# Kernel optimization log

Measured on AMD Instinct MI355X. Metric: run time of the kernel, lower is better.

Reference implementation:

```python
import jax, jax.numpy as jnp
import numpy as np

B, T, E = 8, 1024, 1024
H, HS = 16, 64  # num_heads, head_size; H*HS == E


def setup_inputs() -> dict:
    key = jax.random.key(0)
    k1, k2, k3, k4, k5, k6 = jax.random.split(key, 6)
    x = jax.random.normal(k1, (B, T, E), dtype=jnp.float32)
    s = E ** -0.5
    Wk = jax.random.normal(k2, (H, HS, E), dtype=jnp.float32) * s
    Wq = jax.random.normal(k3, (H, HS, E), dtype=jnp.float32) * s
    Wv = jax.random.normal(k4, (H, HS, E), dtype=jnp.float32) * s
    Wproj = jax.random.normal(k5, (E, E), dtype=jnp.float32) * s
    i = 0
    return {"x": x, "Wk": Wk, "Wq": Wq, "Wv": Wv, "Wproj": Wproj, "i": i}


def reference(x, Wk, Wq, Wv, Wproj, i):
    # choices fixed at full supernet config: embed_dim=E, head_size=HS, no biases.
    b, t, e = x.shape
    hs = Wk.shape[1]
    # per-head projections, heads batched: [B,H,T,HS]
    k = jnp.einsum('bte,hde->bhtd', x, Wk)
    q = jnp.einsum('bte,hde->bhtd', x, Wq)
    v = jnp.einsum('bte,hde->bhtd', x, Wv)
    wei = jnp.einsum('bhtd,bhsd->bhts', q, k) * (hs ** -0.5)  # [B,H,T,T]
    causal = jnp.tril(jnp.ones((t, t), dtype=bool))
    wei = jnp.where(causal, wei, -jnp.inf)
    wei = jax.nn.softmax(wei, axis=-1)  # dropout p=0 (eval)
    out = jnp.einsum('bhts,bhsd->bthd', wei, v).reshape(b, t, -1)  # concat heads
    out = out @ Wproj.T  # proj, bias_proj=False
    return out
```

## Files before the change

### kernel.cpp

```cpp
#include <hip/hip_runtime.h>

#define B_  8
#define T_  1024
#define E_  1024
#define H_  16
#define HS_ 64
#define K_  1024

typedef __bf16 bf16x8 __attribute__((ext_vector_type(8)));
typedef float  f32x4  __attribute__((ext_vector_type(4)));
typedef unsigned short us;

__device__ __forceinline__ us f2bf(float f) {
    union { float f; unsigned int i; } c; c.f = f;
    unsigned int x = c.i;
    return (us)((x + 0x7fff + ((x >> 16) & 1)) >> 16);
}
__device__ __forceinline__ us f2bf_t(float f) {
    union { float f; unsigned int i; } c; c.f = f;
    return (us)(c.i >> 16);
}
__device__ __forceinline__ bf16x8 cvt8(const float* p) {
    float4 a = *reinterpret_cast<const float4*>(p);
    float4 b = *reinterpret_cast<const float4*>(p + 4);
    union { bf16x8 v; us u[8]; } c;
    c.u[0] = f2bf(a.x); c.u[1] = f2bf(a.y); c.u[2] = f2bf(a.z); c.u[3] = f2bf(a.w);
    c.u[4] = f2bf(b.x); c.u[5] = f2bf(b.y); c.u[6] = f2bf(b.z); c.u[7] = f2bf(b.w);
    return c.v;
}
__device__ __forceinline__ void async_cp16(const us* g, us* l) {
    __builtin_amdgcn_global_load_lds((const unsigned int*)g, (unsigned int*)l, 16, 0, 0);
}

__global__ __launch_bounds__(256) void cvt_kernel(
    const float* __restrict__ sx, const float* __restrict__ sq,
    const float* __restrict__ sk, const float* __restrict__ sv,
    const float* __restrict__ sp,
    us* __restrict__ dx, us* __restrict__ dq, us* __restrict__ dk,
    us* __restrict__ dv, us* __restrict__ dp)
{
    const int y = blockIdx.y;
    const float* src = (y == 0) ? sx : (y == 1) ? sq : (y == 2) ? sk : (y == 3) ? sv : sp;
    us*          dst = (y == 0) ? dx : (y == 1) ? dq : (y == 2) ? dk : (y == 3) ? dv : dp;
    const size_t n = (y == 0) ? (size_t)B_ * T_ * E_ : (size_t)E_ * E_;
    const size_t i = ((size_t)blockIdx.x * 256 + threadIdx.x) * 8;
    if (i >= n) return;
    *reinterpret_cast<bf16x8*>(dst + i) = cvt8(src + i);
}

__global__ __launch_bounds__(256) void qkv_gf(
    const us* __restrict__ A,
    const us* __restrict__ Wq, const us* __restrict__ Wk, const us* __restrict__ Wv,
    us* __restrict__ q, us* __restrict__ k, us* __restrict__ vT)
{
    const int type = blockIdx.z;
    const us* Bm = (type == 0) ? Wq : (type == 1) ? Wk : Wv;
    us* out      = (type == 0) ? q  : (type == 1) ? k  : vT;
    const int vtrans = (type == 2);

    __shared__ __align__(16) us As[128 * 64];
    __shared__ __align__(16) us Bs[128 * 64];

    const int tid  = threadIdx.x;
    const int lane = tid & 63;
    const int w    = tid >> 6;
    const int quad = lane >> 4;
    const int l15  = lane & 15;
    const int wm   = w >> 1, wn = w & 1;
    const int row0 = blockIdx.x * 128;
    const int col0 = blockIdx.y * 128;
    const int x7   = l15 & 7;
    const int ca0  = (quad ^ x7) * 8;
    const int ca1  = ((4 + quad) ^ x7) * 8;

    const us* pa[4]; const us* pb[4];
#pragma unroll
    for (int i = 0; i < 4; ++i) {
        const int idx = tid + i * 256;
        const int r   = idx >> 3;
        const int c8  = ((idx & 7) ^ (r & 7)) * 8;
        pa[i] = A  + (size_t)(row0 + r) * K_ + c8;
        pb[i] = Bm + (size_t)(col0 + r) * K_ + c8;
    }

    f32x4 acc[4][4] = {};
    for (int k0 = 0; k0 < K_; k0 += 64) {
        __syncthreads();
#pragma unroll
        for (int i = 0; i < 4; ++i) {
            async_cp16(pa[i], &As[(tid + i * 256) * 8]);
            async_cp16(pb[i], &Bs[(tid + i * 256) * 8]);
            pa[i] += 64; pb[i] += 64;
        }
        __syncthreads();
#pragma unroll
        for (int kk = 0; kk < 2; ++kk) {
            const int ca = kk ? ca1 : ca0;
            bf16x8 af[4], bf[4];
#pragma unroll
            for (int t = 0; t < 4; ++t) {
                af[t] = *reinterpret_cast<const bf16x8*>(&As[(wm * 64 + t * 16 + l15) * 64 + ca]);
                bf[t] = *reinterpret_cast<const bf16x8*>(&Bs[(wn * 64 + t * 16 + l15) * 64 + ca]);
            }
#pragma unroll
            for (int mt = 0; mt < 4; ++mt)
#pragma unroll
                for (int nt = 0; nt < 4; ++nt)
                    acc[mt][nt] = __builtin_amdgcn_mfma_f32_16x16x32_bf16(af[mt], bf[nt], acc[mt][nt], 0, 0, 0);
        }
    }

#pragma unroll
    for (int mt = 0; mt < 4; ++mt)
#pragma unroll
        for (int nt = 0; nt < 4; ++nt)
#pragma unroll
            for (int r = 0; r < 4; ++r) {
                const int m = row0 + wm * 64 + mt * 16 + quad * 4 + r;
                const int n = col0 + wn * 64 + nt * 16 + l15;
                const int b = m >> 10, t = m & 1023;
                const int h = n >> 6,  d = n & 63;
                const us vb = f2bf(acc[mt][nt][r]);
                if (vtrans)  out[((size_t)((b * 16 + h) * 64 + d)) * 1024 + t] = vb;
                else         out[((size_t)(b * 16 + h) * 1024 + t) * 64 + d] = vb;
            }
}

__global__ __launch_bounds__(256) void proj_gf(
    const us* __restrict__ A, const us* __restrict__ Bm, float* __restrict__ C)
{
    __shared__ __align__(16) us As[128 * 64];
    __shared__ __align__(16) us Bs[128 * 64];

    const int tid  = threadIdx.x;
    const int lane = tid & 63;
    const int w    = tid >> 6;
    const int quad = lane >> 4;
    const int l15  = lane & 15;
    const int wm   = w >> 1, wn = w & 1;
    const int row0 = blockIdx.x * 128;
    const int col0 = blockIdx.y * 128;
    const int x7   = l15 & 7;
    const int ca0  = (quad ^ x7) * 8;
    const int ca1  = ((4 + quad) ^ x7) * 8;

    const us* pa[4]; const us* pb[4];
#pragma unroll
    for (int i = 0; i < 4; ++i) {
        const int idx = tid + i * 256;
        const int r   = idx >> 3;
        const int c8  = ((idx & 7) ^ (r & 7)) * 8;
        pa[i] = A  + (size_t)(row0 + r) * K_ + c8;
        pb[i] = Bm + (size_t)(col0 + r) * K_ + c8;
    }

    f32x4 acc[4][4] = {};
    for (int k0 = 0; k0 < K_; k0 += 64) {
        __syncthreads();
#pragma unroll
        for (int i = 0; i < 4; ++i) {
            async_cp16(pa[i], &As[(tid + i * 256) * 8]);
            async_cp16(pb[i], &Bs[(tid + i * 256) * 8]);
            pa[i] += 64; pb[i] += 64;
        }
        __syncthreads();
#pragma unroll
        for (int kk = 0; kk < 2; ++kk) {
            const int ca = kk ? ca1 : ca0;
            bf16x8 af[4], bf[4];
#pragma unroll
            for (int t = 0; t < 4; ++t) {
                af[t] = *reinterpret_cast<const bf16x8*>(&As[(wm * 64 + t * 16 + l15) * 64 + ca]);
                bf[t] = *reinterpret_cast<const bf16x8*>(&Bs[(wn * 64 + t * 16 + l15) * 64 + ca]);
            }
#pragma unroll
            for (int mt = 0; mt < 4; ++mt)
#pragma unroll
                for (int nt = 0; nt < 4; ++nt)
                    acc[mt][nt] = __builtin_amdgcn_mfma_f32_16x16x32_bf16(af[mt], bf[nt], acc[mt][nt], 0, 0, 0);
        }
    }

#pragma unroll
    for (int mt = 0; mt < 4; ++mt)
#pragma unroll
        for (int nt = 0; nt < 4; ++nt)
#pragma unroll
            for (int r = 0; r < 4; ++r) {
                const int m = row0 + wm * 64 + mt * 16 + quad * 4 + r;
                const int n = col0 + wn * 64 + nt * 16 + l15;
                C[(size_t)m * E_ + n] = acc[mt][nt][r];
            }
}

#define CSCALE 0.18033688011112042f

__global__ __launch_bounds__(256) void attn_v8(
    const us* __restrict__ Q, const us* __restrict__ K,
    const us* __restrict__ VT, us* __restrict__ O)
{
    const int px = blockIdx.x;
    const int bh = blockIdx.y;
    const int tA = px, tB = 15 - px;
    const size_t base  = (size_t)bh * T_ * HS_;
    const size_t baseT = (size_t)bh * HS_ * T_;
    const int tid  = threadIdx.x;
    const int w    = tid >> 6;
    const int lane = tid & 63;
    const int quad = lane >> 4;
    const int l15  = lane & 15;

    __shared__ __align__(16) us kt[64][72];
    __shared__ __align__(16) us vt[64][72];
    __shared__ __align__(16) us psA[4][16][72];
    __shared__ __align__(16) us psB[4][16][72];

    const int rowA = tA * 64 + w * 16;
    const int rowB = tB * 64 + w * 16;

    bf16x8 qfA0, qfA1, qfB0, qfB1;
    {
        const us* qa = Q + base + (size_t)(rowA + l15) * HS_ + quad * 8;
        const us* qb = Q + base + (size_t)(rowB + l15) * HS_ + quad * 8;
        qfA0 = *reinterpret_cast<const bf16x8*>(qa);
        qfA1 = *reinterpret_cast<const bf16x8*>(qa + 32);
        qfB0 = *reinterpret_cast<const bf16x8*>(qb);
        qfB1 = *reinterpret_cast<const bf16x8*>(qb + 32);
    }

    const int sr0 = tid >> 3;
    const int sc0 = (tid & 7) * 8;
    const int sr1 = sr0 + 32;

    const us* kp0 = K + base + (size_t)sr0 * HS_ + sc0;
    const us* kp1 = K + base + (size_t)sr1 * HS_ + sc0;
    const us* vp0 = VT + baseT + (size_t)sr0 * T_ + sc0;
    const us* vp1 = VT + baseT + (size_t)sr1 * T_ + sc0;

    float lA[4] = {0.f, 0.f, 0.f, 0.f}, lB[4] = {0.f, 0.f, 0.f, 0.f};
    f32x4 oA[4] = {}, oB[4] = {};

    bf16x8 kr0, kr1, vr0, vr1;
    kr0 = *reinterpret_cast<const bf16x8*>(kp0);
    kr1 = *reinterpret_cast<const bf16x8*>(kp1);
    vr0 = *reinterpret_cast<const bf16x8*>(vp0);
    vr1 = *reinterpret_cast<const bf16x8*>(vp1);

    const int nch = tB + 1;
    for (int ch = 0; ch < nch; ++ch) {
        const int s0 = ch * 64;
        const bool actA = (ch <= tA);

        __syncthreads();
        *reinterpret_cast<bf16x8*>(&kt[sr0][sc0]) = kr0;
        *reinterpret_cast<bf16x8*>(&kt[sr1][sc0]) = kr1;
        *reinterpret_cast<bf16x8*>(&vt[sr0][sc0]) = vr0;
        *reinterpret_cast<bf16x8*>(&vt[sr1][sc0]) = vr1;
        __syncthreads();

        if (ch + 1 < nch) {
            kp0 += 64 * HS_; kp1 += 64 * HS_; vp0 += 64; vp1 += 64;
            kr0 = *reinterpret_cast<const bf16x8*>(kp0);
            kr1 = *reinterpret_cast<const bf16x8*>(kp1);
            vr0 = *reinterpret_cast<const bf16x8*>(vp0);
            vr1 = *reinterpret_cast<const bf16x8*>(vp1);
        }

        f32x4 sA[4] = {}, sB[4] = {};
#pragma unroll
        for (int nt = 0; nt < 4; ++nt) {
            bf16x8 kf0 = *reinterpret_cast<const bf16x8*>(&kt[nt * 16 + l15][quad * 8]);
            bf16x8 kf1 = *reinterpret_cast<const bf16x8*>(&kt[nt * 16 + l15][quad * 8 + 32]);
            sB[nt] = __builtin_amdgcn_mfma_f32_16x16x32_bf16(qfB0, kf0, sB[nt], 0, 0, 0);
            sB[nt] = __builtin_amdgcn_mfma_f32_16x16x32_bf16(qfB1, kf1, sB[nt], 0, 0, 0);
            if (actA) {
                sA[nt] = __builtin_amdgcn_mfma_f32_16x16x32_bf16(qfA0, kf0, sA[nt], 0, 0, 0);
                sA[nt] = __builtin_amdgcn_mfma_f32_16x16x32_bf16(qfA1, kf1, sA[nt], 0, 0, 0);
            }
        }
        if (ch == tB) {
#pragma unroll
            for (int nt = 0; nt < 4; ++nt)
#pragma unroll
                for (int r = 0; r < 4; ++r)
                    if (s0 + nt * 16 + l15 > rowB + quad * 4 + r) sB[nt][r] = -1e30f;
        }
        if (ch == tA) {
#pragma unroll
            for (int nt = 0; nt < 4; ++nt)
#pragma unroll
                for (int r = 0; r < 4; ++r)
                    if (s0 + nt * 16 + l15 > rowA + quad * 4 + r) sA[nt][r] = -1e30f;
        }

#pragma unroll
        for (int r = 0; r < 4; ++r)
#pragma unroll
            for (int nt = 0; nt < 4; ++nt) {
                const float pB = exp2f(sB[nt][r] * CSCALE);
                lB[r] += pB;
                psB[w][quad * 4 + r][nt * 16 + l15] = f2bf_t(pB);
            }
        if (actA) {
#pragma unroll
            for (int r = 0; r < 4; ++r)
#pragma unroll
                for (int nt = 0; nt < 4; ++nt) {
                    const float pA = exp2f(sA[nt][r] * CSCALE);
                    lA[r] += pA;
                    psA[w][quad * 4 + r][nt * 16 + l15] = f2bf_t(pA);
                }
        }

        bf16x8 pfB0 = *reinterpret_cast<const bf16x8*>(&psB[w][l15][quad * 8]);
        bf16x8 pfB1 = *reinterpret_cast<const bf16x8*>(&psB[w][l15][quad * 8 + 32]);
        bf16x8 pfA0, pfA1;
        if (actA) {
            pfA0 = *reinterpret_cast<const bf16x8*>(&psA[w][l15][quad * 8]);
            pfA1 = *reinterpret_cast<const bf16x8*>(&psA[w][l15][quad * 8 + 32]);
        }

#pragma unroll
        for (int dt = 0; dt < 4; ++dt) {
            bf16x8 vf0 = *reinterpret_cast<const bf16x8*>(&vt[dt * 16 + l15][quad * 8]);
            bf16x8 vf1 = *reinterpret_cast<const bf16x8*>(&vt[dt * 16 + l15][quad * 8 + 32]);
            oB[dt] = __builtin_amdgcn_mfma_f32_16x16x32_bf16(pfB0, vf0, oB[dt], 0, 0, 0);
            oB[dt] = __builtin_amdgcn_mfma_f32_16x16x32_bf16(pfB1, vf1, oB[dt], 0, 0, 0);
            if (actA) {
                oA[dt] = __builtin_amdgcn_mfma_f32_16x16x32_bf16(pfA0, vf0, oA[dt], 0, 0, 0);
                oA[dt] = __builtin_amdgcn_mfma_f32_16x16x32_bf16(pfA1, vf1, oA[dt], 0, 0, 0);
            }
        }
    }

#pragma unroll
    for (int r = 0; r < 4; ++r) {
#pragma unroll
        for (int off = 1; off < 16; off <<= 1) {
            lA[r] += __shfl_xor(lA[r], off);
            lB[r] += __shfl_xor(lB[r], off);
        }
    }
    const int b = bh >> 4, h = bh & 15;
#pragma unroll
    for (int r = 0; r < 4; ++r) {
        const float invA = 1.f / lA[r];
        const float invB = 1.f / lB[r];
        const size_t offA = ((size_t)b * T_ + rowA + quad * 4 + r) * E_ + h * HS_;
        const size_t offB = ((size_t)b * T_ + rowB + quad * 4 + r) * E_ + h * HS_;
#pragma unroll
        for (int dt = 0; dt < 4; ++dt) {
            O[offA + dt * 16 + l15] = f2bf(oA[dt][r] * invA);
            O[offB + dt * 16 + l15] = f2bf(oB[dt][r] * invB);
        }
    }
}

extern "C" void kernel_launch(void* const* d_in, const int* in_sizes, int n_in,
                              void* d_out, int out_size, void* d_ws, size_t ws_size,
                              hipStream_t stream) {
    const float* x  = (const float*)d_in[0];
    const float* Wk = (const float*)d_in[1];
    const float* Wq = (const float*)d_in[2];
    const float* Wv = (const float*)d_in[3];
    const float* Wp = (const float*)d_in[4];

    const size_t qe = (size_t)B_ * H_ * T_ * HS_;
    const size_t we = (size_t)E_ * E_;

    us* xb = (us*)d_ws;
    us* wq = xb + qe;
    us* wk = wq + we;
    us* wv = wk + we;
    us* wp = wv + we;
    us* q  = wp + we;
    us* k  = q + qe;
    us* vT = k + qe;
    us* o  = xb;

    cvt_kernel<<<dim3(4096, 5), 256, 0, stream>>>(x, Wq, Wk, Wv, Wp,
                                                  xb, wq, wk, wv, wp);
    qkv_gf<<<dim3(64, 8, 3), 256, 0, stream>>>(xb, wq, wk, wv, q, k, vT);
    attn_v8<<<dim3(8, 128), 256, 0, stream>>>(q, k, vT, o);
    proj_gf<<<dim3(64, 8), 256, 0, stream>>>(o, wp, (float*)d_out);
}
```

Measured before the change: 246.8 us.

## Double-buffer shared memory tiles in QKV and projection GEMMs

Both GEMM kernels now use two shared-memory buffers per operand. Each iteration issues async copies for the next K-tile into the alternate buffer before computing MFMAs on the current one, with a single barrier per iteration instead of two. This aims to hide global-load latency behind compute. Shared memory per block doubles to 64 KB, which may lower occupancy. Correctness depends on the async copy being complete at the barrier.

```diff
diff --git a/kernel.cpp b/kernel.cpp
--- a/kernel.cpp
+++ b/kernel.cpp
@@ -58,8 +58,8 @@
     us* out      = (type == 0) ? q  : (type == 1) ? k  : vT;
     const int vtrans = (type == 2);
 
-    __shared__ __align__(16) us As[128 * 64];
-    __shared__ __align__(16) us Bs[128 * 64];
+    __shared__ __align__(16) us As[2][128 * 64];
+    __shared__ __align__(16) us Bs[2][128 * 64];
 
     const int tid  = threadIdx.x;
     const int lane = tid & 63;
@@ -84,23 +84,32 @@
     }
 
     f32x4 acc[4][4] = {};
-    for (int k0 = 0; k0 < K_; k0 += 64) {
-        __syncthreads();
-#pragma unroll
-        for (int i = 0; i < 4; ++i) {
-            async_cp16(pa[i], &As[(tid + i * 256) * 8]);
-            async_cp16(pb[i], &Bs[(tid + i * 256) * 8]);
-            pa[i] += 64; pb[i] += 64;
-        }
-        __syncthreads();
+#pragma unroll
+    for (int i = 0; i < 4; ++i) {
+        async_cp16(pa[i], &As[0][(tid + i * 256) * 8]);
+        async_cp16(pb[i], &Bs[0][(tid + i * 256) * 8]);
+        pa[i] += 64; pb[i] += 64;
+    }
+    __syncthreads();
+
+    for (int t = 0; t < 16; ++t) {
+        const int cur = t & 1;
+        if (t < 15) {
+#pragma unroll
+            for (int i = 0; i < 4; ++i) {
+                async_cp16(pa[i], &As[cur ^ 1][(tid + i * 256) * 8]);
+                async_cp16(pb[i], &Bs[cur ^ 1][(tid + i * 256) * 8]);
+                pa[i] += 64; pb[i] += 64;
+            }
+        }
 #pragma unroll
         for (int kk = 0; kk < 2; ++kk) {
             const int ca = kk ? ca1 : ca0;
             bf16x8 af[4], bf[4];
 #pragma unroll
-            for (int t = 0; t < 4; ++t) {
-                af[t] = *reinterpret_cast<const bf16x8*>(&As[(wm * 64 + t * 16 + l15) * 64 + ca]);
-                bf[t] = *reinterpret_cast<const bf16x8*>(&Bs[(wn * 64 + t * 16 + l15) * 64 + ca]);
+            for (int tt = 0; tt < 4; ++tt) {
+                af[tt] = *reinterpret_cast<const bf16x8*>(&As[cur][(wm * 64 + tt * 16 + l15) * 64 + ca]);
+                bf[tt] = *reinterpret_cast<const bf16x8*>(&Bs[cur][(wn * 64 + tt * 16 + l15) * 64 + ca]);
             }
 #pragma unroll
             for (int mt = 0; mt < 4; ++mt)
@@ -108,6 +117,7 @@
                 for (int nt = 0; nt < 4; ++nt)
                     acc[mt][nt] = __builtin_amdgcn_mfma_f32_16x16x32_bf16(af[mt], bf[nt], acc[mt][nt], 0, 0, 0);
         }
+        __syncthreads();
     }
 
 #pragma unroll
@@ -129,8 +139,8 @@
 __global__ __launch_bounds__(256) void proj_gf(
     const us* __restrict__ A, const us* __restrict__ Bm, float* __restrict__ C)
 {
-    __shared__ __align__(16) us As[128 * 64];
-    __shared__ __align__(16) us Bs[128 * 64];
+    __shared__ __align__(16) us As[2][128 * 64];
+    __shared__ __align__(16) us Bs[2][128 * 64];
 
     const int tid  = threadIdx.x;
     const int lane = tid & 63;
@@ -155,23 +165,32 @@
     }
 
     f32x4 acc[4][4] = {};
-    for (int k0 = 0; k0 < K_; k0 += 64) {
-        __syncthreads();
-#pragma unroll
-        for (int i = 0; i < 4; ++i) {
-            async_cp16(pa[i], &As[(tid + i * 256) * 8]);
-            async_cp16(pb[i], &Bs[(tid + i * 256) * 8]);
-            pa[i] += 64; pb[i] += 64;
-        }
-        __syncthreads();
+#pragma unroll
+    for (int i = 0; i < 4; ++i) {
+        async_cp16(pa[i], &As[0][(tid + i * 256) * 8]);
+        async_cp16(pb[i], &Bs[0][(tid + i * 256) * 8]);
+        pa[i] += 64; pb[i] += 64;
+    }
+    __syncthreads();
+
+    for (int t = 0; t < 16; ++t) {
+        const int cur = t & 1;
+        if (t < 15) {
+#pragma unroll
+            for (int i = 0; i < 4; ++i) {
+                async_cp16(pa[i], &As[cur ^ 1][(tid + i * 256) * 8]);
+                async_cp16(pb[i], &Bs[cur ^ 1][(tid + i * 256) * 8]);
+                pa[i] += 64; pb[i] += 64;
+            }
+        }
 #pragma unroll
         for (int kk = 0; kk < 2; ++kk) {
             const int ca = kk ? ca1 : ca0;
             bf16x8 af[4], bf[4];
 #pragma unroll
-            for (int t = 0; t < 4; ++t) {
-                af[t] = *reinterpret_cast<const bf16x8*>(&As[(wm * 64 + t * 16 + l15) * 64 + ca]);
-                bf[t] = *reinterpret_cast<const bf16x8*>(&Bs[(wn * 64 + t * 16 + l15) * 64 + ca]);
+            for (int tt = 0; tt < 4; ++tt) {
+                af[tt] = *reinterpret_cast<const bf16x8*>(&As[cur][(wm * 64 + tt * 16 + l15) * 64 + ca]);
+                bf[tt] = *reinterpret_cast<const bf16x8*>(&Bs[cur][(wn * 64 + tt * 16 + l15) * 64 + ca]);
             }
 #pragma unroll
             for (int mt = 0; mt < 4; ++mt)
@@ -179,6 +198,7 @@
                 for (int nt = 0; nt < 4; ++nt)
                     acc[mt][nt] = __builtin_amdgcn_mfma_f32_16x16x32_bf16(af[mt], bf[nt], acc[mt][nt], 0, 0, 0);
         }
+        __syncthreads();
     }
 
 #pragma unroll
```

Result: slower. 254.4 us (+3.1%).

## Keep softmax probabilities in registers by computing transposed scores

Applied to the files above, without the earlier changes.

The QK^T MFMA operands are swapped so each lane holds S^T. The exponentiated probabilities then already sit in the A-operand layout of a 16x16x16 bf16 MFMA for the PV product. This removes the per-warp shared-memory P buffers, along with their store and reload, and the mask and row-sum reduction are adapted to the transposed layout. In exchange, PV uses twice as many narrower K=16 MFMAs and more, smaller V fragment loads from LDS, which may cost matrix-core throughput.

```diff
diff --git a/kernel.cpp b/kernel.cpp
--- a/kernel.cpp
+++ b/kernel.cpp
@@ -8,6 +8,7 @@
 #define K_  1024
 
 typedef __bf16 bf16x8 __attribute__((ext_vector_type(8)));
+typedef __bf16 bf16x4 __attribute__((ext_vector_type(4)));
 typedef float  f32x4  __attribute__((ext_vector_type(4)));
 typedef unsigned short us;
 
@@ -30,6 +31,21 @@
 }
 __device__ __forceinline__ void async_cp16(const us* g, us* l) {
     __builtin_amdgcn_global_load_lds((const unsigned int*)g, (unsigned int*)l, 16, 0, 0);
+}
+
+__device__ __forceinline__ f32x4 mfma_pv16(bf16x4 a, bf16x4 b, f32x4 c) {
+#if __has_builtin(__builtin_amdgcn_mfma_f32_16x16x16_bf16)
+    return __builtin_amdgcn_mfma_f32_16x16x16_bf16(a, b, c, 0, 0, 0);
+#elif __has_builtin(__builtin_amdgcn_mfma_f32_16x16x16bf16_1k)
+    typedef short s16x4 __attribute__((ext_vector_type(4)));
+    union U { bf16x4 b; s16x4 s; };
+    U ua, ub; ua.b = a; ub.b = b;
+    return __builtin_amdgcn_mfma_f32_16x16x16bf16_1k(ua.s, ub.s, c, 0, 0, 0);
+#else
+    f32x4 d = c;
+    asm("v_mfma_f32_16x16x16_bf16 %0, %1, %2, %0" : "+v"(d) : "v"(a), "v"(b));
+    return d;
+#endif
 }
 
 __global__ __launch_bounds__(256) void cvt_kernel(
@@ -195,7 +211,7 @@
 
 #define CSCALE 0.18033688011112042f
 
-__global__ __launch_bounds__(256) void attn_v8(
+__global__ __launch_bounds__(256) void attn_v9(
     const us* __restrict__ Q, const us* __restrict__ K,
     const us* __restrict__ VT, us* __restrict__ O)
 {
@@ -212,8 +228,6 @@
 
     __shared__ __align__(16) us kt[64][72];
     __shared__ __align__(16) us vt[64][72];
-    __shared__ __align__(16) us psA[4][16][72];
-    __shared__ __align__(16) us psB[4][16][72];
 
     const int rowA = tA * 64 + w * 16;
     const int rowB = tB * 64 + w * 16;
@@ -237,7 +251,7 @@
     const us* vp0 = VT + baseT + (size_t)sr0 * T_ + sc0;
     const us* vp1 = VT + baseT + (size_t)sr1 * T_ + sc0;
 
-    float lA[4] = {0.f, 0.f, 0.f, 0.f}, lB[4] = {0.f, 0.f, 0.f, 0.f};
+    float lA = 0.f, lB = 0.f;
     f32x4 oA[4] = {}, oB[4] = {};
 
     bf16x8 kr0, kr1, vr0, vr1;
@@ -271,11 +285,11 @@
         for (int nt = 0; nt < 4; ++nt) {
             bf16x8 kf0 = *reinterpret_cast<const bf16x8*>(&kt[nt * 16 + l15][quad * 8]);
             bf16x8 kf1 = *reinterpret_cast<const bf16x8*>(&kt[nt * 16 + l15][quad * 8 + 32]);
-            sB[nt] = __builtin_amdgcn_mfma_f32_16x16x32_bf16(qfB0, kf0, sB[nt], 0, 0, 0);
-            sB[nt] = __builtin_amdgcn_mfma_f32_16x16x32_bf16(qfB1, kf1, sB[nt], 0, 0, 0);
+            sB[nt] = __builtin_amdgcn_mfma_f32_16x16x32_bf16(kf0, qfB0, sB[nt], 0, 0, 0);
+            sB[nt] = __builtin_amdgcn_mfma_f32_16x16x32_bf16(kf1, qfB1, sB[nt], 0, 0, 0);
             if (actA) {
-                sA[nt] = __builtin_amdgcn_mfma_f32_16x16x32_bf16(qfA0, kf0, sA[nt], 0, 0, 0);
-                sA[nt] = __builtin_amdgcn_mfma_f32_16x16x32_bf16(qfA1, kf1, sA[nt], 0, 0, 0);
+                sA[nt] = __builtin_amdgcn_mfma_f32_16x16x32_bf16(kf0, qfA0, sA[nt], 0, 0, 0);
+                sA[nt] = __builtin_amdgcn_mfma_f32_16x16x32_bf16(kf1, qfA1, sA[nt], 0, 0, 0);
             }
         }
         if (ch == tB) {
@@ -283,69 +297,63 @@
             for (int nt = 0; nt < 4; ++nt)
 #pragma unroll
                 for (int r = 0; r < 4; ++r)
-                    if (s0 + nt * 16 + l15 > rowB + quad * 4 + r) sB[nt][r] = -1e30f;
+                    if (s0 + nt * 16 + quad * 4 + r > rowB + l15) sB[nt][r] = -1e30f;
         }
         if (ch == tA) {
 #pragma unroll
             for (int nt = 0; nt < 4; ++nt)
 #pragma unroll
                 for (int r = 0; r < 4; ++r)
-                    if (s0 + nt * 16 + l15 > rowA + quad * 4 + r) sA[nt][r] = -1e30f;
-        }
-
-#pragma unroll
-        for (int r = 0; r < 4; ++r)
+                    if (s0 + nt * 16 + quad * 4 + r > rowA + l15) sA[nt][r] = -1e30f;
+        }
+
+        bf16x4 paB[4], paA[4];
+#pragma unroll
+        for (int nt = 0; nt < 4; ++nt) {
+            union { bf16x4 v; us u[4]; } pk;
+#pragma unroll
+            for (int r = 0; r < 4; ++r) {
+                const float p = exp2f(sB[nt][r] * CSCALE);
+                lB += p;
+                pk.u[r] = f2bf_t(p);
+            }
+            paB[nt] = pk.v;
+        }
+        if (actA) {
 #pragma unroll
             for (int nt = 0; nt < 4; ++nt) {
-                const float pB = exp2f(sB[nt][r] * CSCALE);
-                lB[r] += pB;
-                psB[w][quad * 4 + r][nt * 16 + l15] = f2bf_t(pB);
-            }
-        if (actA) {
-#pragma unroll
-            for (int r = 0; r < 4; ++r)
-#pragma unroll
-                for (int nt = 0; nt < 4; ++nt) {
-                    const float pA = exp2f(sA[nt][r] * CSCALE);
-                    lA[r] += pA;
-                    psA[w][quad * 4 + r][nt * 16 + l15] = f2bf_t(pA);
+                union { bf16x4 v; us u[4]; } pk;
+#pragma unroll
+                for (int r = 0; r < 4; ++r) {
+                    const float p = exp2f(sA[nt][r] * CSCALE);
+                    lA += p;
+                    pk.u[r] = f2bf_t(p);
                 }
-        }
-
-        bf16x8 pfB0 = *reinterpret_cast<const bf16x8*>(&psB[w][l15][quad * 8]);
-        bf16x8 pfB1 = *reinterpret_cast<const bf16x8*>(&psB[w][l15][quad * 8 + 32]);
-        bf16x8 pfA0, pfA1;
-        if (actA) {
-            pfA0 = *reinterpret_cast<const bf16x8*>(&psA[w][l15][quad * 8]);
-            pfA1 = *reinterpret_cast<const bf16x8*>(&psA[w][l15][quad * 8 + 32]);
+                paA[nt] = pk.v;
+            }
         }
 
 #pragma unroll
         for (int dt = 0; dt < 4; ++dt) {
-            bf16x8 vf0 = *reinterpret_cast<const bf16x8*>(&vt[dt * 16 + l15][quad * 8]);
-            bf16x8 vf1 = *reinterpret_cast<const bf16x8*>(&vt[dt * 16 + l15][quad * 8 + 32]);
-            oB[dt] = __builtin_amdgcn_mfma_f32_16x16x32_bf16(pfB0, vf0, oB[dt], 0, 0, 0);
-            oB[dt] = __builtin_amdgcn_mfma_f32_16x16x32_bf16(pfB1, vf1, oB[dt], 0, 0, 0);
-            if (actA) {
-                oA[dt] = __builtin_amdgcn_mfma_f32_16x16x32_bf16(pfA0, vf0, oA[dt], 0, 0, 0);
-                oA[dt] = __builtin_amdgcn_mfma_f32_16x16x32_bf16(pfA1, vf1, oA[dt], 0, 0, 0);
-            }
-        }
-    }
-
+#pragma unroll
+            for (int nt = 0; nt < 4; ++nt) {
+                const bf16x4 vf = *reinterpret_cast<const bf16x4*>(
+                    &vt[dt * 16 + l15][nt * 16 + quad * 4]);
+                oB[dt] = mfma_pv16(paB[nt], vf, oB[dt]);
+                if (actA) oA[dt] = mfma_pv16(paA[nt], vf, oA[dt]);
+            }
+        }
+    }
+
+    lA += __shfl_xor(lA, 16); lA += __shfl_xor(lA, 32);
+    lB += __shfl_xor(lB, 16); lB += __shfl_xor(lB, 32);
+
+    const int b = bh >> 4, h = bh & 15;
 #pragma unroll
     for (int r = 0; r < 4; ++r) {
-#pragma unroll
-        for (int off = 1; off < 16; off <<= 1) {
-            lA[r] += __shfl_xor(lA[r], off);
-            lB[r] += __shfl_xor(lB[r], off);
-        }
-    }
-    const int b = bh >> 4, h = bh & 15;
-#pragma unroll
-    for (int r = 0; r < 4; ++r) {
-        const float invA = 1.f / lA[r];
-        const float invB = 1.f / lB[r];
+        const int src = (lane & 48) + quad * 4 + r;
+        const float invA = 1.f / __shfl(lA, src);
+        const float invB = 1.f / __shfl(lB, src);
         const size_t offA = ((size_t)b * T_ + rowA + quad * 4 + r) * E_ + h * HS_;
         const size_t offB = ((size_t)b * T_ + rowB + quad * 4 + r) * E_ + h * HS_;
 #pragma unroll
@@ -381,6 +389,6 @@
     cvt_kernel<<<dim3(4096, 5), 256, 0, stream>>>(x, Wq, Wk, Wv, Wp,
                                                   xb, wq, wk, wv, wp);
     qkv_gf<<<dim3(64, 8, 3), 256, 0, stream>>>(xb, wq, wk, wv, q, k, vT);
-    attn_v8<<<dim3(8, 128), 256, 0, stream>>>(q, k, vT, o);
+    attn_v9<<<dim3(8, 128), 256, 0, stream>>>(q, k, vT, o);
     proj_gf<<<dim3(64, 8), 256, 0, stream>>>(o, wp, (float*)d_out);
 }
```

Result: no change. 250.8 us (+1.6%).
